# Optimization experiments

Hardware: AMD Instinct MI355X
Metric: run time of the kernel (lower is better)

Reference implementation:

```python
import jax, jax.numpy as jnp
import numpy as np

B, T, E, K, NNEG = 128, 512, 128, 4, 64


def setup_inputs() -> dict:
    key = jax.random.key(0)
    k1, k2, k3, k4 = jax.random.split(key, 4)
    base_payload = jax.random.normal(k1, (B, T, E), dtype=jnp.float32)
    mapped_ctx_payload = jax.random.normal(k2, (B, T, E, K), dtype=jnp.float32)
    seq_lens = jax.random.randint(k3, (B,), 1, T + 1, dtype=jnp.int32)
    # valid positions mask over the flattened (B*T) pool of possible negatives
    valid = (jnp.arange(T)[None, :] < seq_lens[:, None]).reshape(-1)  # [B*T]
    logits = jnp.where(valid, 0.0, -1e30)[None, :]                    # [1, B*T]
    logits = jnp.broadcast_to(logits, (B, B * T))
    # mirrors torch.multinomial(mask, n_negatives): one draw set per batch row
    sample_ids = jax.random.categorical(k4, logits, shape=(NNEG, B)).T.astype(jnp.int32)
    return {
        "base_payload": base_payload,
        "mapped_ctx_payload": mapped_ctx_payload,
        "seq_lens": seq_lens,
        "sample_ids": sample_ids,
    }


def reference(base_payload, mapped_ctx_payload, seq_lens, sample_ids):
    b, t, e = base_payload.shape
    n_steps = mapped_ctx_payload.shape[-1]
    # length mask [b, t]
    len_mask = (jnp.arange(t)[None, :] < seq_lens[:, None]).astype(base_payload.dtype)
    # zero context embeddings past each sequence's length
    trimmed_mce = mapped_ctx_payload * len_mask[:, :, None, None]  # [b, t, e, n_steps]
    # gather sampled negatives from the flattened base embedding pool
    neg_samples = base_payload.reshape(b * t, e)[sample_ids]  # [b, n_neg, e]

    step_losses = []
    for i in range(1, n_steps + 1):
        ce_i = trimmed_mce[:, : t - i, :, i - 1]   # [b, t-i, e]
        be_i = base_payload[:, i:]                  # [b, t-i, e]
        positive_pred = jnp.sum(ce_i * be_i, axis=-1)             # [b, t-i]
        neg_pred = jnp.einsum('bse,bne->bsn', ce_i, neg_samples)  # [b, t-i, n_neg]
        logits = jnp.concatenate([positive_pred[..., None], neg_pred], axis=-1)
        step_losses.append(-jax.nn.log_softmax(logits, axis=-1)[:, :, 0].mean())
    return jnp.stack(step_losses).mean()
```

## Files before the change

kernel.cpp:

```cpp
#include <hip/hip_runtime.h>
#include <math.h>

#define NB 128
#define NT 512
#define NE 128
#define NK 4
#define NNEG 64
#define SCHUNK 32
#define APITCH 33
#define BPITCH 68


__global__ void zero_out_k(float* out) { *out = 0.f; }

__launch_bounds__(256, 3)
__global__ void cpc_kernel(const float* __restrict__ base,
                           const float* __restrict__ mce,
                           const int*  __restrict__ seq_lens,
                           const int*  __restrict__ sample_ids,
                           float* __restrict__ out)
{
    const int b  = blockIdx.y;
    const int s0 = blockIdx.x * SCHUNK;
    const int L  = seq_lens[b];
    const float LOG65 = 4.1743873f;
    const float wgt[4] = {1.f/261632.f, 1.f/261120.f, 1.f/260608.f, 1.f/260096.f};

    if (s0 >= L) {
        if (threadIdx.x == 0) {
            float c = 0.f;
            #pragma unroll
            for (int i = 1; i <= NK; ++i) {
                int hi = min(SCHUNK, (NT - i) - s0);
                if (hi > 0) c += (float)hi * LOG65 * wgt[i - 1];
            }
            atomicAdd(out, c);
        }
        return;
    }

    __shared__ float4 Ash[SCHUNK * APITCH];
    __shared__ float  Bsh[NE * BPITCH];

    const int tid  = threadIdx.x;
    const int wave = tid >> 6;
    const int lane = tid & 63;
    const int mg   = lane >> 4;
    const int ng   = lane & 15;
    const int half = lane >> 5;
    const int el   = lane & 31;
    const int sw   = s0 + wave * 8;

    const float4* mce4 = (const float4*)mce;

    {
        const int e  = tid & 127;
        const int nh = tid >> 7;
        #pragma unroll 4
        for (int it = 0; it < 32; ++it) {
            int n = it * 2 + nh;
            int r = sample_ids[b * NNEG + n];
            Bsh[e * BPITCH + n] = base[r * NE + e];
        }
    }

    float acc[2][4][4];
    #pragma unroll
    for (int d = 0; d < 2; ++d)
        #pragma unroll
        for (int k = 0; k < 4; ++k)
            #pragma unroll
            for (int j = 0; j < 4; ++j) acc[d][k][j] = 0.f;

    float pp[4][4];
    #pragma unroll
    for (int j = 0; j < 4; ++j)
        #pragma unroll
        for (int k = 0; k < 4; ++k) pp[j][k] = 0.f;

    for (int ep = 0; ep < 4; ++ep) {
        if (ep) __syncthreads();
        {
            const int e_l = tid & 31;
            const int sl0 = tid >> 5;
            #pragma unroll
            for (int r = 0; r < 4; ++r) {
                int sl = sl0 + 8 * r;
                Ash[sl * APITCH + e_l] =
                    mce4[(b * NT + s0 + sl) * NE + ep * 32 + e_l];
            }
        }
        __syncthreads();

        {
            const float4* Arow0 = &Ash[(wave * 8 + 2 * mg    ) * APITCH];
            const float4* Arow1 = &Ash[(wave * 8 + 2 * mg + 1) * APITCH];
            const float*  Bcol  = &Bsh[ep * 32 * BPITCH + 4 * ng];
            #pragma unroll 4
            for (int e = 0; e < 32; ++e) {
                float4 a0 = Arow0[e];
                float4 a1 = Arow1[e];
                float4 bv = *(const float4*)(Bcol + e * BPITCH);
                const float* a0f = reinterpret_cast<const float*>(&a0);
                const float* a1f = reinterpret_cast<const float*>(&a1);
                const float* bvf = reinterpret_cast<const float*>(&bv);
                #pragma unroll
                for (int k = 0; k < 4; ++k) {
                    float v0 = a0f[k], v1 = a1f[k];
                    #pragma unroll
                    for (int j = 0; j < 4; ++j) {
                        acc[0][k][j] = fmaf(v0, bvf[j], acc[0][k][j]);
                        acc[1][k][j] = fmaf(v1, bvf[j], acc[1][k][j]);
                    }
                }
            }
        }

        {
            const int eg = ep * 32 + el;
            #pragma unroll
            for (int j = 0; j < 4; ++j) {
                int srow = wave * 8 + 4 * half + j;
                int sg   = s0 + srow;
                float4 av = Ash[srow * APITCH + el];
                const float* af = reinterpret_cast<const float*>(&av);
                #pragma unroll
                for (int i = 1; i <= 4; ++i) {
                    int row = min(sg + i, NT - 1);
                    float bb = base[(b * NT + row) * NE + eg];
                    pp[j][i - 1] = fmaf(af[i - 1], bb, pp[j][i - 1]);
                }
            }
        }
    }

    #pragma unroll
    for (int j = 0; j < 4; ++j)
        #pragma unroll
        for (int k = 0; k < 4; ++k) {
            float v = pp[j][k];
            v += __shfl_xor(v, 1);
            v += __shfl_xor(v, 2);
            v += __shfl_xor(v, 4);
            v += __shfl_xor(v, 8);
            v += __shfl_xor(v, 16);
            pp[j][k] = v;
        }

    float lossacc = 0.f;
    #pragma unroll
    for (int d = 0; d < 2; ++d) {
        int s = sw + 2 * mg + d;
        bool unm = (s < L);
        int jj = 2 * (mg & 1) + d;
        #pragma unroll
        for (int k = 0; k < 4; ++k) {
            if (s < NT - (k + 1)) {
                float p  = pp[jj][k];
                float z0 = acc[d][k][0], z1 = acc[d][k][1];
                float z2 = acc[d][k][2], z3 = acc[d][k][3];
                float m = fmaxf(fmaxf(z0, z1), fmaxf(z2, z3));
                m = fmaxf(m, __shfl_xor(m, 1));
                m = fmaxf(m, __shfl_xor(m, 2));
                m = fmaxf(m, __shfl_xor(m, 4));
                m = fmaxf(m, __shfl_xor(m, 8));
                m = fmaxf(m, p);
                float ssum = __expf(z0 - m) + __expf(z1 - m)
                           + __expf(z2 - m) + __expf(z3 - m);
                ssum += __shfl_xor(ssum, 1);
                ssum += __shfl_xor(ssum, 2);
                ssum += __shfl_xor(ssum, 4);
                ssum += __shfl_xor(ssum, 8);
                ssum += __expf(p - m);
                float loss = __logf(ssum) + (m - p);
                loss = unm ? loss : LOG65;
                lossacc += wgt[k] * loss;
            }
        }
    }
    lossacc += __shfl_xor(lossacc, 16);
    lossacc += __shfl_xor(lossacc, 32);
    if (lane == 0) atomicAdd(out, lossacc);
}

extern "C" void kernel_launch(void* const* d_in, const int* in_sizes, int n_in,
                              void* d_out, int out_size, void* d_ws, size_t ws_size,
                              hipStream_t stream) {
    (void)in_sizes; (void)n_in; (void)out_size; (void)d_ws; (void)ws_size;
    const float* base       = (const float*)d_in[0];
    const float* mce        = (const float*)d_in[1];
    const int*   seq_lens   = (const int*)d_in[2];
    const int*   sample_ids = (const int*)d_in[3];
    float* out = (float*)d_out;

    zero_out_k<<<1, 1, 0, stream>>>(out);
    dim3 grid(NT / SCHUNK, NB);
    cpc_kernel<<<grid, 256, 0, stream>>>(base, mce, seq_lens, sample_ids, out);
}
```

Before: 264.7 us.

## Compute negative logits with bf16 MFMA instead of fp32 FMA loops

The fp32 register-tiled FMA matmul for negative scores becomes bf16 MFMA 16x16x32 instructions. The whole 32x128x4 context chunk is loaded once into swizzled LDS fragments, which replaces the four-pass e-chunk loop. Positive dot products are computed from the same bf16 fragments and passed through LDS. This removes several barriers and much FMA work, but drops the input precision to bf16 and adds conversion cost during the load.

Result: faster. 251.3 us (-5.1%).

```diff
diff --git a/kernel.cpp b/kernel.cpp
--- a/kernel.cpp
+++ b/kernel.cpp
@@ -3,22 +3,21 @@
 
 #define NB 128
 #define NT 512
-#define NE 128
-#define NK 4
+#define NEDIM 128
 #define NNEG 64
 #define SCHUNK 32
-#define APITCH 33
-#define BPITCH 68
 
+typedef __bf16 bf16x8 __attribute__((ext_vector_type(8)));
+typedef float  f32x4  __attribute__((ext_vector_type(4)));
 
 __global__ void zero_out_k(float* out) { *out = 0.f; }
 
 __launch_bounds__(256, 3)
-__global__ void cpc_kernel(const float* __restrict__ base,
-                           const float* __restrict__ mce,
-                           const int*  __restrict__ seq_lens,
-                           const int*  __restrict__ sample_ids,
-                           float* __restrict__ out)
+__global__ void cpc_mfma_kernel(const float* __restrict__ base,
+                                const float* __restrict__ mce,
+                                const int*  __restrict__ seq_lens,
+                                const int*  __restrict__ sample_ids,
+                                float* __restrict__ out)
 {
     const int b  = blockIdx.y;
     const int s0 = blockIdx.x * SCHUNK;
@@ -30,7 +29,7 @@
         if (threadIdx.x == 0) {
             float c = 0.f;
             #pragma unroll
-            for (int i = 1; i <= NK; ++i) {
+            for (int i = 1; i <= 4; ++i) {
                 int hi = min(SCHUNK, (NT - i) - s0);
                 if (hi > 0) c += (float)hi * LOG65 * wgt[i - 1];
             }
@@ -39,143 +38,140 @@
         return;
     }
 
-    __shared__ float4 Ash[SCHUNK * APITCH];
-    __shared__ float  Bsh[NE * BPITCH];
+    __shared__ __bf16 Afrag[2048 * 8];
+    __shared__ __bf16 Bfrag[1024 * 8];
+    __shared__ float  pos_lds[128];
 
     const int tid  = threadIdx.x;
-    const int wave = tid >> 6;
     const int lane = tid & 63;
-    const int mg   = lane >> 4;
-    const int ng   = lane & 15;
-    const int half = lane >> 5;
-    const int el   = lane & 31;
-    const int sw   = s0 + wave * 8;
+    const int w    = tid >> 6;
+    const int q    = lane >> 4;
+    const int fl   = lane & 15;
 
     const float4* mce4 = (const float4*)mce;
 
-    {
-        const int e  = tid & 127;
-        const int nh = tid >> 7;
-        #pragma unroll 4
-        for (int it = 0; it < 32; ++it) {
-            int n = it * 2 + nh;
-            int r = sample_ids[b * NNEG + n];
-            Bsh[e * BPITCH + n] = base[r * NE + e];
+    #pragma unroll
+    for (int it = 0; it < 2; ++it) {
+        int g  = tid + 256 * it;
+        int s  = g & 31;
+        int eb = g >> 5;
+        const float4* src = mce4 + (size_t)(b * NT + s0 + s) * NEDIM + eb * 8;
+        float4 v[8];
+        #pragma unroll
+        for (int u = 0; u < 8; ++u) v[u] = src[u];
+        const float* vf = (const float*)v;
+        int Cs = (eb >> 2) * 8 + (s >> 2);
+        int base_chunk = Cs * 64 + (eb & 3) * 16 + (s & 3) * 4;
+        int x = Cs & 7;
+        #pragma unroll
+        for (int k = 0; k < 4; ++k) {
+            int phys = (base_chunk + k) ^ x;
+            bf16x8 o;
+            #pragma unroll
+            for (int u = 0; u < 8; ++u) o[u] = (__bf16)vf[4 * u + k];
+            *(bf16x8*)(&Afrag[phys * 8]) = o;
         }
     }
 
-    float acc[2][4][4];
-    #pragma unroll
-    for (int d = 0; d < 2; ++d)
+    {
+        int n = tid & 63;
+        int r = sample_ids[b * NNEG + n];
+        const float4* srcb = (const float4*)(base + (size_t)r * NEDIM);
+        int eb0 = (tid >> 6) * 4;
         #pragma unroll
-        for (int k = 0; k < 4; ++k)
+        for (int it = 0; it < 4; ++it) {
+            int eb = eb0 + it;
+            float4 v0 = srcb[eb * 2], v1 = srcb[eb * 2 + 1];
+            const float* f0 = (const float*)&v0;
+            const float* f1 = (const float*)&v1;
+            bf16x8 o;
             #pragma unroll
-            for (int j = 0; j < 4; ++j) acc[d][k][j] = 0.f;
-
-    float pp[4][4];
-    #pragma unroll
-    for (int j = 0; j < 4; ++j)
-        #pragma unroll
-        for (int k = 0; k < 4; ++k) pp[j][k] = 0.f;
-
-    for (int ep = 0; ep < 4; ++ep) {
-        if (ep) __syncthreads();
-        {
-            const int e_l = tid & 31;
-            const int sl0 = tid >> 5;
-            #pragma unroll
-            for (int r = 0; r < 4; ++r) {
-                int sl = sl0 + 8 * r;
-                Ash[sl * APITCH + e_l] =
-                    mce4[(b * NT + s0 + sl) * NE + ep * 32 + e_l];
-            }
-        }
-        __syncthreads();
-
-        {
-            const float4* Arow0 = &Ash[(wave * 8 + 2 * mg    ) * APITCH];
-            const float4* Arow1 = &Ash[(wave * 8 + 2 * mg + 1) * APITCH];
-            const float*  Bcol  = &Bsh[ep * 32 * BPITCH + 4 * ng];
-            #pragma unroll 4
-            for (int e = 0; e < 32; ++e) {
-                float4 a0 = Arow0[e];
-                float4 a1 = Arow1[e];
-                float4 bv = *(const float4*)(Bcol + e * BPITCH);
-                const float* a0f = reinterpret_cast<const float*>(&a0);
-                const float* a1f = reinterpret_cast<const float*>(&a1);
-                const float* bvf = reinterpret_cast<const float*>(&bv);
-                #pragma unroll
-                for (int k = 0; k < 4; ++k) {
-                    float v0 = a0f[k], v1 = a1f[k];
-                    #pragma unroll
-                    for (int j = 0; j < 4; ++j) {
-                        acc[0][k][j] = fmaf(v0, bvf[j], acc[0][k][j]);
-                        acc[1][k][j] = fmaf(v1, bvf[j], acc[1][k][j]);
-                    }
-                }
-            }
-        }
-
-        {
-            const int eg = ep * 32 + el;
-            #pragma unroll
-            for (int j = 0; j < 4; ++j) {
-                int srow = wave * 8 + 4 * half + j;
-                int sg   = s0 + srow;
-                float4 av = Ash[srow * APITCH + el];
-                const float* af = reinterpret_cast<const float*>(&av);
-                #pragma unroll
-                for (int i = 1; i <= 4; ++i) {
-                    int row = min(sg + i, NT - 1);
-                    float bb = base[(b * NT + row) * NE + eg];
-                    pp[j][i - 1] = fmaf(af[i - 1], bb, pp[j][i - 1]);
-                }
-            }
+            for (int u = 0; u < 4; ++u) { o[u] = (__bf16)f0[u]; o[4 + u] = (__bf16)f1[u]; }
+            *(bf16x8*)(&Bfrag[(eb * 64 + n) * 8]) = o;
         }
     }
+    __syncthreads();
+
+    f32x4 acc[2][4];
+    #pragma unroll
+    for (int mtl = 0; mtl < 2; ++mtl)
+        #pragma unroll
+        for (int nt = 0; nt < 4; ++nt) acc[mtl][nt] = (f32x4){0.f, 0.f, 0.f, 0.f};
 
     #pragma unroll
-    for (int j = 0; j < 4; ++j)
+    for (int kstep = 0; kstep < 4; ++kstep) {
+        bf16x8 af[2];
         #pragma unroll
-        for (int k = 0; k < 4; ++k) {
-            float v = pp[j][k];
-            v += __shfl_xor(v, 1);
-            v += __shfl_xor(v, 2);
-            v += __shfl_xor(v, 4);
-            v += __shfl_xor(v, 8);
-            v += __shfl_xor(v, 16);
-            pp[j][k] = v;
+        for (int mtl = 0; mtl < 2; ++mtl) {
+            int Cs = kstep * 8 + (2 * w + mtl);
+            int phys = (Cs * 64 + lane) ^ (Cs & 7);
+            af[mtl] = *(const bf16x8*)(&Afrag[phys * 8]);
         }
+        bf16x8 bv[4];
+        #pragma unroll
+        for (int nt = 0; nt < 4; ++nt) {
+            int cB = (kstep * 4 + q) * 64 + nt * 16 + fl;
+            bv[nt] = *(const bf16x8*)(&Bfrag[cB * 8]);
+        }
+        #pragma unroll
+        for (int mtl = 0; mtl < 2; ++mtl)
+            #pragma unroll
+            for (int nt = 0; nt < 4; ++nt)
+                acc[mtl][nt] = __builtin_amdgcn_mfma_f32_16x16x32_bf16(
+                    af[mtl], bv[nt], acc[mtl][nt], 0, 0, 0);
+    }
+
+    {
+        int m    = tid >> 1;
+        int eh   = tid & 1;
+        int sloc = m >> 2, ip = (m & 3) + 1;
+        int srow = s0 + sloc + ip; if (srow > NT - 1) srow = NT - 1;
+        const float* brow = base + (size_t)(b * NT + srow) * NEDIM + eh * 64;
+        int mt = m >> 4, flm = m & 15;
+        float psum = 0.f;
+        #pragma unroll
+        for (int el = 0; el < 8; ++el) {
+            int eb = eh * 8 + el;
+            int Cs = (eb >> 2) * 8 + mt;
+            int phys = (Cs * 64 + (eb & 3) * 16 + flm) ^ (Cs & 7);
+            bf16x8 av = *(const bf16x8*)(&Afrag[phys * 8]);
+            #pragma unroll
+            for (int u = 0; u < 8; ++u)
+                psum = fmaf((float)av[u], brow[el * 8 + u], psum);
+        }
+        psum += __shfl_xor(psum, 1);
+        if (eh == 0) pos_lds[m] = psum;
+    }
+    __syncthreads();
 
     float lossacc = 0.f;
     #pragma unroll
-    for (int d = 0; d < 2; ++d) {
-        int s = sw + 2 * mg + d;
-        bool unm = (s < L);
-        int jj = 2 * (mg & 1) + d;
+    for (int mtl = 0; mtl < 2; ++mtl) {
         #pragma unroll
-        for (int k = 0; k < 4; ++k) {
-            if (s < NT - (k + 1)) {
-                float p  = pp[jj][k];
-                float z0 = acc[d][k][0], z1 = acc[d][k][1];
-                float z2 = acc[d][k][2], z3 = acc[d][k][3];
-                float m = fmaxf(fmaxf(z0, z1), fmaxf(z2, z3));
-                m = fmaxf(m, __shfl_xor(m, 1));
-                m = fmaxf(m, __shfl_xor(m, 2));
-                m = fmaxf(m, __shfl_xor(m, 4));
-                m = fmaxf(m, __shfl_xor(m, 8));
-                m = fmaxf(m, p);
-                float ssum = __expf(z0 - m) + __expf(z1 - m)
-                           + __expf(z2 - m) + __expf(z3 - m);
-                ssum += __shfl_xor(ssum, 1);
-                ssum += __shfl_xor(ssum, 2);
-                ssum += __shfl_xor(ssum, 4);
-                ssum += __shfl_xor(ssum, 8);
-                ssum += __expf(p - m);
-                float loss = __logf(ssum) + (m - p);
-                loss = unm ? loss : LOG65;
-                lossacc += wgt[k] * loss;
-            }
+        for (int r = 0; r < 4; ++r) {
+            int m  = w * 32 + mtl * 16 + q * 4 + r;
+            int sg = s0 + (m >> 2);
+            int ip = (m & 3) + 1;
+            float z0 = acc[mtl][0][r], z1 = acc[mtl][1][r];
+            float z2 = acc[mtl][2][r], z3 = acc[mtl][3][r];
+            float p  = pos_lds[m];
+            float mx = fmaxf(fmaxf(z0, z1), fmaxf(z2, z3));
+            mx = fmaxf(mx, __shfl_xor(mx, 1));
+            mx = fmaxf(mx, __shfl_xor(mx, 2));
+            mx = fmaxf(mx, __shfl_xor(mx, 4));
+            mx = fmaxf(mx, __shfl_xor(mx, 8));
+            mx = fmaxf(mx, p);
+            float es = __expf(z0 - mx) + __expf(z1 - mx)
+                     + __expf(z2 - mx) + __expf(z3 - mx);
+            es += __shfl_xor(es, 1);
+            es += __shfl_xor(es, 2);
+            es += __shfl_xor(es, 4);
+            es += __shfl_xor(es, 8);
+            es += __expf(p - mx);
+            float loss = __logf(es) + (mx - p);
+            loss = (sg < L) ? loss : LOG65;
+            bool take = (sg < NT - ip) && (fl == 0);
+            lossacc += take ? wgt[ip - 1] * loss : 0.f;
         }
     }
     lossacc += __shfl_xor(lossacc, 16);
@@ -195,5 +191,5 @@
 
     zero_out_k<<<1, 1, 0, stream>>>(out);
     dim3 grid(NT / SCHUNK, NB);
-    cpc_kernel<<<grid, 256, 0, stream>>>(base, mce, seq_lens, sample_ids, out);
+    cpc_mfma_kernel<<<grid, 256, 0, stream>>>(base, mce, seq_lens, sample_ids, out);
 }
```
